# Kernel tuning notes

Measured on AMD Instinct MI355X. Metric: run time of the kernel, lower is better.

The kernel has to match this reference:

```python
import jax, jax.numpy as jnp
import numpy as np

B, N, C = 8, 8192, 64
P, K = 2048, 16
C_IN = 2 * C + 6   # 134: concat(diff, center) of (feat ++ xyz)
H1, H2 = 64, 128
EPS = 1e-5


def setup_inputs() -> dict:
    key = jax.random.key(0)
    ks = jax.random.split(key, 16)
    inp = {
        "xyz": jax.random.normal(ks[0], (B, N, 3), dtype=jnp.float32),
        "feat": jax.random.normal(ks[1], (B, C, N), dtype=jnp.float32),
        # SharedMLP layer 1: 1x1 conv + BN(eval) + ReLU
        "W1": jax.random.normal(ks[2], (H1, C_IN), dtype=jnp.float32) * (1.0 / np.sqrt(C_IN)),
        "b1": jnp.zeros((H1,), dtype=jnp.float32),
        "g1": jax.random.uniform(ks[3], (H1,), minval=0.5, maxval=1.5, dtype=jnp.float32),
        "be1": jax.random.normal(ks[4], (H1,), dtype=jnp.float32) * 0.1,
        "m1": jax.random.normal(ks[5], (H1,), dtype=jnp.float32) * 0.1,
        "v1": jax.random.uniform(ks[6], (H1,), minval=0.5, maxval=1.5, dtype=jnp.float32),
        # SharedMLP layer 2
        "W2": jax.random.normal(ks[7], (H2, H1), dtype=jnp.float32) * (1.0 / np.sqrt(H1)),
        "b2": jnp.zeros((H2,), dtype=jnp.float32),
        "g2": jax.random.uniform(ks[8], (H2,), minval=0.5, maxval=1.5, dtype=jnp.float32),
        "be2": jax.random.normal(ks[9], (H2,), dtype=jnp.float32) * 0.1,
        "m2": jax.random.normal(ks[10], (H2,), dtype=jnp.float32) * 0.1,
        "v2": jax.random.uniform(ks[11], (H2,), minval=0.5, maxval=1.5, dtype=jnp.float32),
        "npoints": P,
    }
    return inp


def _mlp_layer(x, W, b, g, be, m, v):
    # x: [b,p,k,cin] -> 1x1 conv (einsum) + eval-mode BN + ReLU
    y = jnp.einsum("bpkc,oc->bpko", x, W) + b
    y = g * (y - m) * jax.lax.rsqrt(v + EPS) + be
    return jax.nn.relu(y)


def reference(xyz, feat, W1, b1, g1, be1, m1, v1, W2, b2, g2, be2, m2, v2, npoints):
    p = npoints
    # Range sampling: take first p points
    new_xyz = xyz[:, :p]                       # [b,p,3]
    feat_t = jnp.swapaxes(feat, 1, 2)          # [b,n,c]
    feat_x = jnp.concatenate([feat_t, xyz], axis=-1)   # [b,n,c+3] (use_xyz)
    new_feat_x = feat_x[:, :p]                 # [b,p,c+3]
    # KNN via squared euclidean distance, expanded form to avoid [b,p,n,3]
    sq_q = jnp.sum(new_xyz * new_xyz, axis=-1)           # [b,p]
    sq_r = jnp.sum(xyz * xyz, axis=-1)                   # [b,n]
    dots = jnp.einsum("bpd,bnd->bpn", new_xyz, xyz)      # [b,p,n]
    d2 = sq_q[:, :, None] + sq_r[:, None, :] - 2.0 * dots
    _, idx = jax.lax.top_k(-d2, K)             # [b,p,k] nearest (ascending dist)
    # Gather neighbor features: [b,p,k,c+3]
    knn_feat = jax.vmap(lambda f, i: f[i])(feat_x, idx)
    tiled = jnp.broadcast_to(new_feat_x[:, :, None, :], knn_feat.shape)
    edge = jnp.concatenate([knn_feat - tiled, tiled], axis=-1)  # [b,p,k,2c+6]
    h = _mlp_layer(edge, W1, b1, g1, be1, m1, v1)
    h = _mlp_layer(h, W2, b2, g2, be2, m2, v2)              # [b,p,k,H2]
    new_feat = jnp.swapaxes(jnp.max(h, axis=2), 1, 2)       # [b,H2,p]
    sample_idx = jnp.broadcast_to(jnp.arange(p, dtype=jnp.int32), (xyz.shape[0], p))
    return new_xyz, new_feat, sample_idx
```

## Files before the change

### kernel.cpp

```cpp
#include <hip/hip_runtime.h>
#include <hip/hip_bf16.h>

#define BB 8
#define NN 8192
#define CC 64
#define PP 2048
#define KK 16
#define H1 64
#define H2 128
#define K1PAD 160
#define K2PAD 72

typedef float  f32x4 __attribute__((ext_vector_type(4)));
typedef short  s16x8 __attribute__((ext_vector_type(8)));

#define OFF_FXT   0u
#define OFF_PTS4  17825792u
#define OFF_KNN   19922944u
#define OFF_W1P   20971520u
#define OFF_W2P   20992000u
#define OFF_C1    21010432u
#define OFF_C2    21010688u

static __device__ __forceinline__ unsigned short bf16b(float v) {
    __hip_bfloat16 h = __float2bfloat16(v);
    return *reinterpret_cast<unsigned short*>(&h);
}
static __device__ __forceinline__ unsigned pk2(float a, float b) {
    return ((unsigned)bf16b(b) << 16) | (unsigned)bf16b(a);
}

__global__ void k0_weights(const float* __restrict__ W1, const float* __restrict__ b1,
                           const float* __restrict__ g1, const float* __restrict__ be1,
                           const float* __restrict__ m1, const float* __restrict__ v1,
                           const float* __restrict__ W2, const float* __restrict__ b2,
                           const float* __restrict__ g2, const float* __restrict__ be2,
                           const float* __restrict__ m2, const float* __restrict__ v2,
                           unsigned short* __restrict__ w1p, unsigned short* __restrict__ w2p,
                           float* __restrict__ c1, float* __restrict__ c2) {
    int i = blockIdx.x * 256 + threadIdx.x;
    if (i < 64 * K1PAD) {
        int n = i / K1PAD, c = i - n * K1PAD;
        float s = g1[n] * rsqrtf(v1[n] + 1e-5f);
        float val = 0.f;
        if (c < 67)                 val = W1[n * 134 + c] * s;
        else if (c >= 72 && c < 139) val = W1[n * 134 + (c - 5)] * s;
        w1p[i] = bf16b(val);
    }
    int j = i - 64 * K1PAD;
    if (j >= 0 && j < 128 * K2PAD) {
        int o = j / K2PAD, k = j - o * K2PAD;
        float s = g2[o] * rsqrtf(v2[o] + 1e-5f);
        w2p[j] = bf16b((k < 64) ? W2[o * 64 + k] * s : 0.f);
    }
    int l = i - (64 * K1PAD + 128 * K2PAD);
    if (l >= 0 && l < 64) {
        float s = g1[l] * rsqrtf(v1[l] + 1e-5f);
        c1[l] = s * (b1[l] - m1[l]) + be1[l];
    }
    int p = l - 64;
    if (p >= 0 && p < 128) {
        float s = g2[p] * rsqrtf(v2[p] + 1e-5f);
        c2[p] = s * (b2[p] - m2[p]) + be2[p];
    }
}

__global__ __launch_bounds__(512) void k1_prep(const float* __restrict__ xyz,
                                               const float* __restrict__ feat,
                                               float* __restrict__ fxt,
                                               float4* __restrict__ pts4,
                                               float* __restrict__ out0,
                                               float* __restrict__ out2) {
    __shared__ float tile[68][65];
    int b  = blockIdx.x >> 7;
    int n0 = (blockIdx.x & 127) * 64;
    int tx = threadIdx.x & 63, ty = threadIdx.x >> 6;
    for (int c = ty; c < 68; c += 8) {
        float v;
        if (c < 64)       v = feat[((size_t)b * 64 + c) * NN + n0 + tx];
        else if (c < 67)  v = xyz[((size_t)b * NN + n0 + tx) * 3 + (c - 64)];
        else              v = 0.f;
        tile[c][tx] = v;
    }
    __syncthreads();
    size_t base = ((size_t)b * NN + n0) * 68;
    for (int e = threadIdx.x; e < 64 * 68; e += 512) {
        int nl = e / 68, c = e - nl * 68;
        fxt[base + e] = tile[c][nl];
    }
    if (threadIdx.x < 64) {
        int n = n0 + threadIdx.x;
        float x = tile[64][threadIdx.x], y = tile[65][threadIdx.x], z = tile[66][threadIdx.x];
        pts4[(size_t)b * NN + n] = make_float4(x, y, z, x * x + y * y + z * z);
        if (n0 < PP) out2[b * PP + n] = (float)n;
    }
    if (n0 < PP) {
        for (int e = threadIdx.x; e < 64 * 3; e += 512) {
            int nl = e / 3, d = e - nl * 3;
            out0[((size_t)b * PP + n0 + nl) * 3 + d] = tile[64 + d][nl];
        }
    }
}

__global__ __launch_bounds__(1024, 4) void k2_knn(const float4* __restrict__ pts4,
                                                  int* __restrict__ knn) {
    __shared__ float4 stage[8192];
    __shared__ float2 scratch[16][64];
    int lane = threadIdx.x & 63;
    int wv   = threadIdx.x >> 6;
    int b    = blockIdx.x >> 5;
    int q0   = (blockIdx.x & 31) * 64 + wv * 4;
    size_t pb = (size_t)b * NN;

    float4 qc = make_float4(0.f, 0.f, 0.f, 0.f);
    if (lane < 4) qc = pts4[pb + q0 + lane];
    float qx2 = -2.f * qc.x, qy2 = -2.f * qc.y, qz2 = -2.f * qc.z;
    float bx[4], by[4], bz[4];
#pragma unroll
    for (int q = 0; q < 4; ++q) {
        bx[q] = __shfl(qx2, q); by[q] = __shfl(qy2, q); bz[q] = __shfl(qz2, q);
    }

#pragma unroll
    for (int i = 0; i < 8; ++i) {
        int p = i * 1024 + threadIdx.x;
        float4 v = pts4[pb + p];
        int r = p >> 6, c = p & 63;
        stage[(r << 6) | ((c + (r >> 1)) & 63)] = v;
    }
    __syncthreads();

    float m[4];
#pragma unroll
    for (int q = 0; q < 4; ++q) m[q] = 3.402823466e+38f;
#pragma unroll
    for (int rr = 0; rr < 2; ++rr) {
        int rowbase = (2 * lane + rr) << 6;
#pragma unroll
        for (int j8 = 0; j8 < 8; ++j8) {
            float4 cc[8];
#pragma unroll
            for (int i = 0; i < 8; ++i)
                cc[i] = stage[rowbase | ((j8 * 8 + i + lane) & 63)];
#pragma unroll
            for (int q = 0; q < 4; ++q) {
                float x = bx[q], y = by[q], z = bz[q];
#pragma unroll
                for (int i = 0; i < 8; i += 2) {
                    float e0 = fmaf(z, cc[i].z, fmaf(y, cc[i].y, fmaf(x, cc[i].x, cc[i].w)));
                    float e1 = fmaf(z, cc[i+1].z, fmaf(y, cc[i+1].y, fmaf(x, cc[i+1].x, cc[i+1].w)));
                    m[q] = fminf(fminf(m[q], e0), e1);
                }
            }
        }
    }

#pragma unroll 1
    for (int q = 0; q < 4; ++q) {
        float v = m[q];
#pragma unroll
        for (int k = 2; k <= 64; k <<= 1) {
#pragma unroll
            for (int j = k >> 1; j > 0; j >>= 1) {
                float p = __shfl_xor(v, j, 64);
                bool up = ((lane & k) == 0);
                bool lo = ((lane & j) == 0);
                float mn = fminf(v, p), mx = fmaxf(v, p);
                v = (up == lo) ? mn : mx;
            }
        }
        float tq = __shfl(v, 15, 64);

        float x = bx[q], y = by[q], z = bz[q];
        unsigned long long rm = __ballot(m[q] <= tq);
        int cnt = 0;
        unsigned long long below = (lane == 63) ? 0x7FFFFFFFFFFFFFFFull
                                                : ((1ull << lane) - 1ull);
        while (rm) {
            int sl = __ffsll((long long)rm) - 1; rm &= rm - 1;
            int phys = (lane + sl) & 63;
            float4 c0 = stage[((2 * sl) << 6) | phys];
            float4 c1 = stage[((2 * sl + 1) << 6) | phys];
            float e0 = fmaf(z, c0.z, fmaf(y, c0.y, fmaf(x, c0.x, c0.w)));
            float e1 = fmaf(z, c1.z, fmaf(y, c1.y, fmaf(x, c1.x, c1.w)));
            unsigned long long b0 = __ballot(e0 <= tq);
            if (e0 <= tq) {
                int pos = cnt + __popcll(b0 & below);
                if (pos < 64)
                    scratch[wv][pos] = make_float2(e0, __int_as_float(sl * 128 + lane));
            }
            cnt += __popcll(b0);
            unsigned long long b1 = __ballot(e1 <= tq);
            if (e1 <= tq) {
                int pos = cnt + __popcll(b1 & below);
                if (pos < 64)
                    scratch[wv][pos] = make_float2(e1, __int_as_float(sl * 128 + 64 + lane));
            }
            cnt += __popcll(b1);
        }
        __threadfence_block();
        int M = min(cnt, 64);
        float2 kv = scratch[wv][lane];
        float kd = (lane < M) ? kv.x : 3.402823466e+38f;
        int   kn = (lane < M) ? __float_as_int(kv.y) : 0x7FFFFFFF;

#pragma unroll
        for (int k = 2; k <= 64; k <<= 1) {
#pragma unroll
            for (int j = k >> 1; j > 0; j >>= 1) {
                float pd = __shfl_xor(kd, j, 64);
                int   pn = __shfl_xor(kn, j, 64);
                bool takeMin = (((lane & k) == 0) == ((lane & j) == 0));
                bool pLess = (pd < kd) || (pd == kd && pn < kn);
                bool sw = takeMin ? pLess : !pLess;
                kd = sw ? pd : kd;
                kn = sw ? pn : kn;
            }
        }
        if (lane < 16)
            knn[((size_t)(b * PP + q0 + q)) * KK + lane] = kn;
        __threadfence_block();
    }
}

__global__ __launch_bounds__(64, 2) void k3_mlp(const float* __restrict__ fxt,
                                                const int* __restrict__ knn,
                                                const unsigned short* __restrict__ w1p,
                                                const unsigned short* __restrict__ w2p,
                                                const float* __restrict__ c1,
                                                const float* __restrict__ c2,
                                                float* __restrict__ out1) {
    __shared__ __align__(16) char seg[8192];
    int lane = threadIdx.x;
    int wg   = blockIdx.x;
    float4* sh_t4 = (float4*)(seg + 7424);
    unsigned* sh_tbd = (unsigned*)(seg + 7696);
    unsigned short* h1l = (unsigned short*)(seg + 5120);

    int col = lane & 15, quad = lane >> 4;

    s16x8 w1f[5][4];
#pragma unroll
    for (int ks = 0; ks < 5; ++ks)
#pragma unroll
        for (int nt = 0; nt < 4; ++nt)
            w1f[ks][nt] = *(const s16x8*)(w1p + (nt * 16 + col) * K1PAD + ks * 32 + quad * 8);
    s16x8 w2f[2][8];
#pragma unroll
    for (int ks = 0; ks < 2; ++ks)
#pragma unroll
        for (int nt = 0; nt < 8; ++nt)
            w2f[ks][nt] = *(const s16x8*)(w2p + (nt * 16 + col) * K2PAD + ks * 32 + quad * 8);
    float c1v[4], c2v[8];
#pragma unroll
    for (int nt = 0; nt < 4; ++nt) c1v[nt] = c1[nt * 16 + col];
#pragma unroll
    for (int nt = 0; nt < 8; ++nt) c2v[nt] = c2[nt * 16 + col];

    for (int it = 0; it < 8; ++it) {
        int qlin = wg + 2048 * it;
        int b = qlin >> 11, qq = qlin & 2047;
        const float4* fx4 = (const float4*)fxt;
        __syncthreads();
        if (lane < 17) {
            float4 v = fx4[((size_t)b * NN + qq) * 17 + lane];
            sh_t4[lane] = v;
            sh_tbd[lane * 2]     = pk2(v.x, v.y);
            sh_tbd[lane * 2 + 1] = pk2(v.z, v.w);
        }
        __syncthreads();
        {
            int r = lane >> 2, s = lane & 3;
            int nidx = knn[((size_t)b * PP + qq) * KK + r];
            const float4* rowp = fx4 + ((size_t)b * NN + nidx) * 17;
            char* erow = seg + r * 320;
#pragma unroll
            for (int j = 0; j < 5; ++j) {
                int c4 = j * 4 + s;
                if (c4 < 17) {
                    float4 v = rowp[c4], t = sh_t4[c4];
                    *(unsigned*)(erow + c4 * 8)     = pk2(v.x - t.x, v.y - t.y);
                    *(unsigned*)(erow + c4 * 8 + 4) = pk2(v.z - t.z, v.w - t.w);
                }
            }
            for (int j = s; j < 34; j += 4)
                *(unsigned*)(erow + 144 + j * 4) = sh_tbd[j];
#pragma unroll
            for (int j = s; j < 12; j += 4) {
                int w = (j < 2) ? (34 + j) : (68 + j);
                *(unsigned*)(erow + w * 4) = 0u;
            }
        }
        __syncthreads();
        f32x4 acc1[4];
#pragma unroll
        for (int nt = 0; nt < 4; ++nt) acc1[nt] = (f32x4){0.f, 0.f, 0.f, 0.f};
#pragma unroll
        for (int ks = 0; ks < 5; ++ks) {
            s16x8 a = *(const s16x8*)(seg + (lane & 15) * 320 + ks * 64 + quad * 16);
#pragma unroll
            for (int nt = 0; nt < 4; ++nt)
                acc1[nt] = __builtin_amdgcn_mfma_f32_16x16x32_bf16(a, w1f[ks][nt], acc1[nt], 0, 0, 0);
        }
#pragma unroll
        for (int nt = 0; nt < 4; ++nt) {
#pragma unroll
            for (int r = 0; r < 4; ++r) {
                float y = fmaxf(acc1[nt][r] + c1v[nt], 0.f);
                h1l[(quad * 4 + r) * K2PAD + nt * 16 + col] = bf16b(y);
            }
        }
        __syncthreads();
        f32x4 acc2[8];
#pragma unroll
        for (int nt = 0; nt < 8; ++nt) acc2[nt] = (f32x4){0.f, 0.f, 0.f, 0.f};
#pragma unroll
        for (int ks = 0; ks < 2; ++ks) {
            s16x8 a = *(const s16x8*)(seg + 5120 + (lane & 15) * 144 + ks * 64 + quad * 16);
#pragma unroll
            for (int nt = 0; nt < 8; ++nt)
                acc2[nt] = __builtin_amdgcn_mfma_f32_16x16x32_bf16(a, w2f[ks][nt], acc2[nt], 0, 0, 0);
        }
#pragma unroll
        for (int nt = 0; nt < 8; ++nt) {
            float m0 = fmaxf(fmaxf(acc2[nt][0], acc2[nt][1]), fmaxf(acc2[nt][2], acc2[nt][3]));
            m0 = m0 + c2v[nt];
            m0 = fmaxf(m0, 0.f);
            m0 = fmaxf(m0, __shfl_xor(m0, 16, 64));
            m0 = fmaxf(m0, __shfl_xor(m0, 32, 64));
            if (quad == 0)
                out1[((size_t)b * H2 + nt * 16 + col) * PP + qq] = m0;
        }
    }
}

extern "C" void kernel_launch(void* const* d_in, const int* in_sizes, int n_in,
                              void* d_out, int out_size, void* d_ws, size_t ws_size,
                              hipStream_t stream) {
    const float* xyz  = (const float*)d_in[0];
    const float* feat = (const float*)d_in[1];
    const float* W1   = (const float*)d_in[2];
    const float* b1   = (const float*)d_in[3];
    const float* g1   = (const float*)d_in[4];
    const float* be1  = (const float*)d_in[5];
    const float* m1   = (const float*)d_in[6];
    const float* v1   = (const float*)d_in[7];
    const float* W2   = (const float*)d_in[8];
    const float* b2   = (const float*)d_in[9];
    const float* g2   = (const float*)d_in[10];
    const float* be2  = (const float*)d_in[11];
    const float* m2   = (const float*)d_in[12];
    const float* v2   = (const float*)d_in[13];

    char* ws = (char*)d_ws;
    float*          fxt  = (float*)(ws + OFF_FXT);
    float4*         pts4 = (float4*)(ws + OFF_PTS4);
    int*            knn  = (int*)(ws + OFF_KNN);
    unsigned short* w1p  = (unsigned short*)(ws + OFF_W1P);
    unsigned short* w2p  = (unsigned short*)(ws + OFF_W2P);
    float*          c1   = (float*)(ws + OFF_C1);
    float*          c2   = (float*)(ws + OFF_C2);

    float* out0 = (float*)d_out;
    float* out1 = out0 + (size_t)BB * PP * 3;
    float* out2 = out1 + (size_t)BB * H2 * PP;

    hipLaunchKernelGGL(k0_weights, dim3(77), dim3(256), 0, stream,
                       W1, b1, g1, be1, m1, v1, W2, b2, g2, be2, m2, v2,
                       w1p, w2p, c1, c2);
    hipLaunchKernelGGL(k1_prep, dim3(1024), dim3(512), 0, stream,
                       xyz, feat, fxt, pts4, out0, out2);
    hipLaunchKernelGGL(k2_knn, dim3(256), dim3(1024), 0, stream, pts4, knn);
    hipLaunchKernelGGL(k3_mlp, dim3(2048), dim3(64), 0, stream,
                       fxt, knn, w1p, w2p, c1, c2, out1);
}
```

Baseline: 176.1 us.

## Software-pipeline neighbor gathers in MLP kernel and batch KNN bitonic sorts

The MLP kernel now double-buffers neighbor feature rows in registers, prefetching the next iteration's gathered rows while the current one computes. It preloads all KNN indices up front and replaces __syncthreads with LDS waitcnt fences, which is valid only because the workgroup is a single wave. The KNN kernel runs the four threshold bitonic sorts together and handles two queries per final sort pass, giving more independent shuffles for ILP. The cost is higher register pressure and reliance on single-wave execution for LDS ordering.

```diff
diff --git a/kernel.cpp b/kernel.cpp
--- a/kernel.cpp
+++ b/kernel.cpp
@@ -22,6 +22,8 @@
 #define OFF_C1    21010432u
 #define OFF_C2    21010688u
 
+#define FLTMAX 3.402823466e+38f
+
 static __device__ __forceinline__ unsigned short bf16b(float v) {
     __hip_bfloat16 h = __float2bfloat16(v);
     return *reinterpret_cast<unsigned short*>(&h);
@@ -29,6 +31,7 @@
 static __device__ __forceinline__ unsigned pk2(float a, float b) {
     return ((unsigned)bf16b(b) << 16) | (unsigned)bf16b(a);
 }
+#define LDS_FENCE() asm volatile("s_waitcnt lgkmcnt(0)" ::: "memory")
 
 __global__ void k0_weights(const float* __restrict__ W1, const float* __restrict__ b1,
                            const float* __restrict__ g1, const float* __restrict__ be1,
@@ -105,7 +108,7 @@
 __global__ __launch_bounds__(1024, 4) void k2_knn(const float4* __restrict__ pts4,
                                                   int* __restrict__ knn) {
     __shared__ float4 stage[8192];
-    __shared__ float2 scratch[16][64];
+    __shared__ float2 scratch[16][2][64];
     int lane = threadIdx.x & 63;
     int wv   = threadIdx.x >> 6;
     int b    = blockIdx.x >> 5;
@@ -132,7 +135,7 @@
 
     float m[4];
 #pragma unroll
-    for (int q = 0; q < 4; ++q) m[q] = 3.402823466e+38f;
+    for (int q = 0; q < 4; ++q) m[q] = FLTMAX;
 #pragma unroll
     for (int rr = 0; rr < 2; ++rr) {
         int rowbase = (2 * lane + rr) << 6;
@@ -155,71 +158,85 @@
         }
     }
 
-#pragma unroll 1
-    for (int q = 0; q < 4; ++q) {
-        float v = m[q];
+    float sv0 = m[0], sv1 = m[1], sv2 = m[2], sv3 = m[3];
+#pragma unroll
+    for (int k = 2; k <= 64; k <<= 1) {
+#pragma unroll
+        for (int j = k >> 1; j > 0; j >>= 1) {
+            bool keepMin = (((lane & k) == 0) == ((lane & j) == 0));
+            float p0 = __shfl_xor(sv0, j, 64);
+            float p1 = __shfl_xor(sv1, j, 64);
+            float p2 = __shfl_xor(sv2, j, 64);
+            float p3 = __shfl_xor(sv3, j, 64);
+            sv0 = keepMin ? fminf(sv0, p0) : fmaxf(sv0, p0);
+            sv1 = keepMin ? fminf(sv1, p1) : fmaxf(sv1, p1);
+            sv2 = keepMin ? fminf(sv2, p2) : fmaxf(sv2, p2);
+            sv3 = keepMin ? fminf(sv3, p3) : fmaxf(sv3, p3);
+        }
+    }
+    float T[4];
+    T[0] = __shfl(sv0, 15, 64); T[1] = __shfl(sv1, 15, 64);
+    T[2] = __shfl(sv2, 15, 64); T[3] = __shfl(sv3, 15, 64);
+
+    unsigned long long below = (lane == 63) ? 0x7FFFFFFFFFFFFFFFull
+                                            : ((1ull << lane) - 1ull);
+#pragma unroll
+    for (int pr = 0; pr < 4; pr += 2) {
+        float kd[2]; int kn[2];
+#pragma unroll
+        for (int u = 0; u < 2; ++u) {
+            int q = pr + u;
+            float x = bx[q], y = by[q], z = bz[q], tq = T[q];
+            unsigned long long rm = __ballot(m[q] <= tq);
+            int cnt = 0;
+            while (rm) {
+                int sl = __ffsll((long long)rm) - 1; rm &= rm - 1;
+                int phys = (lane + sl) & 63;
+                float4 c0 = stage[((2 * sl) << 6) | phys];
+                float4 c1 = stage[((2 * sl + 1) << 6) | phys];
+                float e0 = fmaf(z, c0.z, fmaf(y, c0.y, fmaf(x, c0.x, c0.w)));
+                float e1 = fmaf(z, c1.z, fmaf(y, c1.y, fmaf(x, c1.x, c1.w)));
+                unsigned long long b0 = __ballot(e0 <= tq);
+                if (e0 <= tq) {
+                    int pos = cnt + __popcll(b0 & below);
+                    if (pos < 64)
+                        scratch[wv][u][pos] = make_float2(e0, __int_as_float(sl * 128 + lane));
+                }
+                cnt += __popcll(b0);
+                unsigned long long b1 = __ballot(e1 <= tq);
+                if (e1 <= tq) {
+                    int pos = cnt + __popcll(b1 & below);
+                    if (pos < 64)
+                        scratch[wv][u][pos] = make_float2(e1, __int_as_float(sl * 128 + 64 + lane));
+                }
+                cnt += __popcll(b1);
+            }
+            LDS_FENCE();
+            int M = min(cnt, 64);
+            float2 kv = scratch[wv][u][lane];
+            kd[u] = (lane < M) ? kv.x : FLTMAX;
+            kn[u] = (lane < M) ? __float_as_int(kv.y) : 0x7FFFFFFF;
+        }
 #pragma unroll
         for (int k = 2; k <= 64; k <<= 1) {
 #pragma unroll
             for (int j = k >> 1; j > 0; j >>= 1) {
-                float p = __shfl_xor(v, j, 64);
-                bool up = ((lane & k) == 0);
-                bool lo = ((lane & j) == 0);
-                float mn = fminf(v, p), mx = fmaxf(v, p);
-                v = (up == lo) ? mn : mx;
+                bool takeMin = (((lane & k) == 0) == ((lane & j) == 0));
+                float pd0 = __shfl_xor(kd[0], j, 64); int pn0 = __shfl_xor(kn[0], j, 64);
+                float pd1 = __shfl_xor(kd[1], j, 64); int pn1 = __shfl_xor(kn[1], j, 64);
+                bool l0 = (pd0 < kd[0]) || (pd0 == kd[0] && pn0 < kn[0]);
+                bool s0 = takeMin ? l0 : !l0;
+                kd[0] = s0 ? pd0 : kd[0]; kn[0] = s0 ? pn0 : kn[0];
+                bool l1 = (pd1 < kd[1]) || (pd1 == kd[1] && pn1 < kn[1]);
+                bool s1 = takeMin ? l1 : !l1;
+                kd[1] = s1 ? pd1 : kd[1]; kn[1] = s1 ? pn1 : kn[1];
             }
         }
-        float tq = __shfl(v, 15, 64);
-
-        float x = bx[q], y = by[q], z = bz[q];
-        unsigned long long rm = __ballot(m[q] <= tq);
-        int cnt = 0;
-        unsigned long long below = (lane == 63) ? 0x7FFFFFFFFFFFFFFFull
-                                                : ((1ull << lane) - 1ull);
-        while (rm) {
-            int sl = __ffsll((long long)rm) - 1; rm &= rm - 1;
-            int phys = (lane + sl) & 63;
-            float4 c0 = stage[((2 * sl) << 6) | phys];
-            float4 c1 = stage[((2 * sl + 1) << 6) | phys];
-            float e0 = fmaf(z, c0.z, fmaf(y, c0.y, fmaf(x, c0.x, c0.w)));
-            float e1 = fmaf(z, c1.z, fmaf(y, c1.y, fmaf(x, c1.x, c1.w)));
-            unsigned long long b0 = __ballot(e0 <= tq);
-            if (e0 <= tq) {
-                int pos = cnt + __popcll(b0 & below);
-                if (pos < 64)
-                    scratch[wv][pos] = make_float2(e0, __int_as_float(sl * 128 + lane));
-            }
-            cnt += __popcll(b0);
-            unsigned long long b1 = __ballot(e1 <= tq);
-            if (e1 <= tq) {
-                int pos = cnt + __popcll(b1 & below);
-                if (pos < 64)
-                    scratch[wv][pos] = make_float2(e1, __int_as_float(sl * 128 + 64 + lane));
-            }
-            cnt += __popcll(b1);
-        }
-        __threadfence_block();
-        int M = min(cnt, 64);
-        float2 kv = scratch[wv][lane];
-        float kd = (lane < M) ? kv.x : 3.402823466e+38f;
-        int   kn = (lane < M) ? __float_as_int(kv.y) : 0x7FFFFFFF;
-
-#pragma unroll
-        for (int k = 2; k <= 64; k <<= 1) {
-#pragma unroll
-            for (int j = k >> 1; j > 0; j >>= 1) {
-                float pd = __shfl_xor(kd, j, 64);
-                int   pn = __shfl_xor(kn, j, 64);
-                bool takeMin = (((lane & k) == 0) == ((lane & j) == 0));
-                bool pLess = (pd < kd) || (pd == kd && pn < kn);
-                bool sw = takeMin ? pLess : !pLess;
-                kd = sw ? pd : kd;
-                kn = sw ? pn : kn;
-            }
-        }
-        if (lane < 16)
-            knn[((size_t)(b * PP + q0 + q)) * KK + lane] = kn;
-        __threadfence_block();
+        if (lane < 16) {
+            knn[((size_t)(b * PP + q0 + pr)) * KK + lane]     = kn[0];
+            knn[((size_t)(b * PP + q0 + pr + 1)) * KK + lane] = kn[1];
+        }
+        LDS_FENCE();
     }
 }
 
@@ -236,8 +253,10 @@
     float4* sh_t4 = (float4*)(seg + 7424);
     unsigned* sh_tbd = (unsigned*)(seg + 7696);
     unsigned short* h1l = (unsigned short*)(seg + 5120);
+    const float4* fx4 = (const float4*)fxt;
 
     int col = lane & 15, quad = lane >> 4;
+    int r = lane >> 2, s = lane & 3;
 
     s16x8 w1f[5][4];
 #pragma unroll
@@ -257,47 +276,62 @@
 #pragma unroll
     for (int nt = 0; nt < 8; ++nt) c2v[nt] = c2[nt * 16 + col];
 
+    int idxA = knn[wg * 16 + (lane >> 4) * 32768 + (lane & 15)];
+    int idxB = knn[wg * 16 + 131072 + (lane >> 4) * 32768 + (lane & 15)];
+
+    float4 cc[2][5];
+    float4 tv[2];
+
+#define PREFETCH(buf, it_) {                                                  \
+        size_t bb_ = (size_t)(it_) * NN;                                      \
+        tv[buf] = make_float4(0.f, 0.f, 0.f, 0.f);                            \
+        if (lane < 17) tv[buf] = fx4[(bb_ + wg) * 17 + lane];                 \
+        int nidx_ = __shfl(((it_) < 4) ? idxA : idxB, ((it_) & 3) * 16 + r, 64); \
+        const float4* rowp_ = fx4 + (bb_ + nidx_) * 17;                       \
+        cc[buf][0] = rowp_[s];      cc[buf][1] = rowp_[4 + s];                \
+        cc[buf][2] = rowp_[8 + s];  cc[buf][3] = rowp_[12 + s];               \
+        cc[buf][4] = rowp_[16];  }
+
+    PREFETCH(0, 0);
+
+#pragma unroll 2
     for (int it = 0; it < 8; ++it) {
-        int qlin = wg + 2048 * it;
-        int b = qlin >> 11, qq = qlin & 2047;
-        const float4* fx4 = (const float4*)fxt;
-        __syncthreads();
+        int cur = it & 1, nxt = cur ^ 1;
         if (lane < 17) {
-            float4 v = fx4[((size_t)b * NN + qq) * 17 + lane];
+            float4 v = tv[cur];
             sh_t4[lane] = v;
             sh_tbd[lane * 2]     = pk2(v.x, v.y);
             sh_tbd[lane * 2 + 1] = pk2(v.z, v.w);
         }
-        __syncthreads();
-        {
-            int r = lane >> 2, s = lane & 3;
-            int nidx = knn[((size_t)b * PP + qq) * KK + r];
-            const float4* rowp = fx4 + ((size_t)b * NN + nidx) * 17;
-            char* erow = seg + r * 320;
-#pragma unroll
-            for (int j = 0; j < 5; ++j) {
-                int c4 = j * 4 + s;
-                if (c4 < 17) {
-                    float4 v = rowp[c4], t = sh_t4[c4];
-                    *(unsigned*)(erow + c4 * 8)     = pk2(v.x - t.x, v.y - t.y);
-                    *(unsigned*)(erow + c4 * 8 + 4) = pk2(v.z - t.z, v.w - t.w);
-                }
-            }
-            for (int j = s; j < 34; j += 4)
-                *(unsigned*)(erow + 144 + j * 4) = sh_tbd[j];
-#pragma unroll
-            for (int j = s; j < 12; j += 4) {
-                int w = (j < 2) ? (34 + j) : (68 + j);
-                *(unsigned*)(erow + w * 4) = 0u;
-            }
-        }
-        __syncthreads();
+        LDS_FENCE();
+        char* erow = seg + r * 320;
+#pragma unroll
+        for (int j = 0; j < 4; ++j) {
+            int c4 = j * 4 + s;
+            float4 v = cc[cur][j], t = sh_t4[c4];
+            *(unsigned*)(erow + c4 * 8)     = pk2(v.x - t.x, v.y - t.y);
+            *(unsigned*)(erow + c4 * 8 + 4) = pk2(v.z - t.z, v.w - t.w);
+        }
+        if (s == 0) {
+            float4 v = cc[cur][4], t = sh_t4[16];
+            *(unsigned*)(erow + 128) = pk2(v.x - t.x, v.y - t.y);
+            *(unsigned*)(erow + 132) = pk2(v.z - t.z, v.w - t.w);
+        }
+        for (int j = s; j < 34; j += 4)
+            *(unsigned*)(erow + 144 + j * 4) = sh_tbd[j];
+#pragma unroll
+        for (int j = s; j < 12; j += 4) {
+            int w = (j < 2) ? (34 + j) : (68 + j);
+            *(unsigned*)(erow + w * 4) = 0u;
+        }
+        if (it < 7) PREFETCH(nxt, it + 1);
+        LDS_FENCE();
         f32x4 acc1[4];
 #pragma unroll
         for (int nt = 0; nt < 4; ++nt) acc1[nt] = (f32x4){0.f, 0.f, 0.f, 0.f};
 #pragma unroll
         for (int ks = 0; ks < 5; ++ks) {
-            s16x8 a = *(const s16x8*)(seg + (lane & 15) * 320 + ks * 64 + quad * 16);
+            s16x8 a = *(const s16x8*)(seg + col * 320 + ks * 64 + quad * 16);
 #pragma unroll
             for (int nt = 0; nt < 4; ++nt)
                 acc1[nt] = __builtin_amdgcn_mfma_f32_16x16x32_bf16(a, w1f[ks][nt], acc1[nt], 0, 0, 0);
@@ -305,18 +339,18 @@
 #pragma unroll
         for (int nt = 0; nt < 4; ++nt) {
 #pragma unroll
-            for (int r = 0; r < 4; ++r) {
-                float y = fmaxf(acc1[nt][r] + c1v[nt], 0.f);
-                h1l[(quad * 4 + r) * K2PAD + nt * 16 + col] = bf16b(y);
+            for (int rr = 0; rr < 4; ++rr) {
+                float y = fmaxf(acc1[nt][rr] + c1v[nt], 0.f);
+                h1l[(quad * 4 + rr) * K2PAD + nt * 16 + col] = bf16b(y);
             }
         }
-        __syncthreads();
+        LDS_FENCE();
         f32x4 acc2[8];
 #pragma unroll
         for (int nt = 0; nt < 8; ++nt) acc2[nt] = (f32x4){0.f, 0.f, 0.f, 0.f};
 #pragma unroll
         for (int ks = 0; ks < 2; ++ks) {
-            s16x8 a = *(const s16x8*)(seg + 5120 + (lane & 15) * 144 + ks * 64 + quad * 16);
+            s16x8 a = *(const s16x8*)(seg + 5120 + col * 144 + ks * 64 + quad * 16);
 #pragma unroll
             for (int nt = 0; nt < 8; ++nt)
                 acc2[nt] = __builtin_amdgcn_mfma_f32_16x16x32_bf16(a, w2f[ks][nt], acc2[nt], 0, 0, 0);
@@ -329,9 +363,10 @@
             m0 = fmaxf(m0, __shfl_xor(m0, 16, 64));
             m0 = fmaxf(m0, __shfl_xor(m0, 32, 64));
             if (quad == 0)
-                out1[((size_t)b * H2 + nt * 16 + col) * PP + qq] = m0;
-        }
-    }
+                out1[((size_t)it * H2 + nt * 16 + col) * PP + wg] = m0;
+        }
+    }
+#undef PREFETCH
 }
 
 extern "C" void kernel_launch(void* const* d_in, const int* in_sizes, int n_in,
```

Result: slower. 185.6 us (+5.4%).
